# Kernel optimization log

Measured on AMD Instinct MI355X. Metric: run time of the kernel, lower is better.

The kernel has to match this reference:

```python
import jax, jax.numpy as jnp
import numpy as np


def setup_inputs() -> dict:
    key = jax.random.key(0)
    k1, k2, k3, k4 = jax.random.split(key, 4)
    B, S, D = 8, 2048, 512
    scale = 1.0 / np.sqrt(D)
    return {
        "x": jax.random.normal(k1, (B, S, D), dtype=jnp.float32),
        "WQ": jax.random.normal(k2, (D, D), dtype=jnp.float32) * scale,
        "WK": jax.random.normal(k3, (D, D), dtype=jnp.float32) * scale,
        "WV": jax.random.normal(k4, (D, D), dtype=jnp.float32) * scale,
    }


def reference(x, WQ, WK, WV):
    # x: [B, S, D]; single-head scaled dot-product self-attention
    Q = jnp.einsum("bsd,de->bse", x, WQ)
    K = jnp.einsum("bsd,de->bse", x, WK)
    V = jnp.einsum("bsd,de->bse", x, WV)
    d_k = jnp.asarray(K.shape[-1], dtype=x.dtype)
    scores = jnp.einsum("bqd,bkd->bqk", Q, K) / jnp.sqrt(d_k)  # [B,S,S]
    weights = jax.nn.softmax(scores, axis=-1)
    return jnp.einsum("bqk,bkd->bqd", weights, V)
```

## Files before the change

### kernel.cpp

```cpp
#include <hip/hip_runtime.h>
#include <cstdint>
#include <cstddef>

#define B_ 8
#define S_ 2048
#define D_ 512

typedef float f32x4 __attribute__((ext_vector_type(4)));
typedef __bf16 bf16x8 __attribute__((ext_vector_type(8)));

__device__ __forceinline__ unsigned short f2bf(float f) {
    unsigned u = __builtin_bit_cast(unsigned, f);
    u += 0x7FFFu + ((u >> 16) & 1u);
    return (unsigned short)(u >> 16);
}

__device__ __forceinline__ void gll16(const void* g, void* l) {
    __builtin_amdgcn_global_load_lds(
        (const __attribute__((address_space(1))) unsigned int*)g,
        (__attribute__((address_space(3))) unsigned int*)l, 16, 0, 0);
}

#define VMCNT(n) asm volatile("s_waitcnt vmcnt(%0)" :: "i"(n) : "memory")
#define SBAR()   __builtin_amdgcn_s_barrier()
#define SCHED0() __builtin_amdgcn_sched_barrier(0)

template<int AMT, int BNT>
__global__ __launch_bounds__(512, 2) void gemm8(
    const unsigned short* __restrict__ A,
    const unsigned short* __restrict__ B,
    void* __restrict__ Cv,
    unsigned short* __restrict__ Cv2,
    float* __restrict__ rs_part,
    int K, int lda, int ldb, int ldc,
    long long sA, long long sB, long long sC,
    float scale, int mode, int ntn, int nbatch)
{
    constexpr int BM     = 64 * AMT;
    constexpr int BN     = 128 * BNT;
    constexpr int ABYTES = BM * 128;
    constexpr int BBYTES = BN * 128;
    constexpr int AH     = ABYTES / 2;
    constexpr int BH     = BBYTES / 2;
    constexpr int AGL    = AMT / 2;
    constexpr int BGL    = BNT;
    constexpr int BUFB   = ABYTES + BBYTES;
    __shared__ __align__(16) char lds[2 * BUFB];

    const int lin = blockIdx.x;
    const int bz  = lin % nbatch;
    const int tq  = lin / nbatch;
    const int tn  = tq % ntn;
    const int tm  = tq / ntn;
    A += (long long)bz * sA;
    B += (long long)bz * sB;
    const int m0   = tm * BM;
    const int n0   = tn * BN;
    const int tid  = threadIdx.x;
    const int lane = tid & 63;
    const int w    = tid >> 6;
    const int g2   = w >> 2;
    const int nb   = w & 3;

    const int lrow = lane >> 3;
    const int swz  = ((lane & 7) ^ lrow) << 3;
    const unsigned short* gA[2][AGL];
    const unsigned short* gB[2][BGL];
    #pragma unroll
    for (int h = 0; h < 2; ++h) {
        #pragma unroll
        for (int i = 0; i < AGL; ++i)
            gA[h][i] = A + (size_t)(m0 + h * (BM / 2) + (w * AGL + i) * 8 + lrow) * lda + swz;
        #pragma unroll
        for (int i = 0; i < BGL; ++i)
            gB[h][i] = B + (size_t)(n0 + h * (BN / 2) + (w * BGL + i) * 8 + lrow) * ldb + swz;
    }
    auto stA = [&](int bs, int h, int kof) {
        #pragma unroll
        for (int i = 0; i < AGL; ++i)
            gll16(gA[h][i] + kof, lds + bs * BUFB + h * AH + (w * AGL + i) * 1024);
    };
    auto stB = [&](int bs, int h, int kof) {
        #pragma unroll
        for (int i = 0; i < BGL; ++i)
            gll16(gB[h][i] + kof, lds + bs * BUFB + ABYTES + h * BH + (w * BGL + i) * 1024);
    };

    const int fr = lane & 15;
    const int gq = lane >> 4;
    const int c0 = (gq ^ (fr & 7)) << 4;
    int aoff[AMT], boff[BNT];
    #pragma unroll
    for (int ml = 0; ml < AMT; ++ml)
        aoff[ml] = (g2 * (16 * AMT) + ml * 16 + fr) * 128 + c0;
    #pragma unroll
    for (int nl = 0; nl < BNT; ++nl)
        boff[nl] = (nb * (16 * BNT) + nl * 16 + fr) * 128 + c0;

    bf16x8 af[2 * AMT], bLO[2 * BNT], bHI[2 * BNT];
    f32x4 acc[2 * AMT][2 * BNT] = {};

    auto ldA = [&](const char* Ab, int mh) {
        #pragma unroll
        for (int ml = 0; ml < AMT; ++ml)
            #pragma unroll
            for (int kk = 0; kk < 2; ++kk)
                af[ml * 2 + kk] = *(const bf16x8*)(Ab + mh * AH + (aoff[ml] ^ (kk << 6)));
    };
    auto ldB = [&](const char* Bb, int nh, bf16x8* bf) {
        #pragma unroll
        for (int nl = 0; nl < BNT; ++nl)
            #pragma unroll
            for (int kk = 0; kk < 2; ++kk)
                bf[nl * 2 + kk] = *(const bf16x8*)(Bb + nh * BH + (boff[nl] ^ (kk << 6)));
    };
    auto mma = [&](int mh, int nh, const bf16x8* bf) {
        __builtin_amdgcn_s_setprio(1);
        #pragma unroll
        for (int ml = 0; ml < AMT; ++ml)
            #pragma unroll
            for (int nl = 0; nl < BNT; ++nl)
                #pragma unroll
                for (int kk = 0; kk < 2; ++kk)
                    acc[mh * AMT + ml][nh * BNT + nl] =
                        __builtin_amdgcn_mfma_f32_16x16x32_bf16(
                            af[ml * 2 + kk], bf[nl * 2 + kk],
                            acc[mh * AMT + ml][nh * BNT + nl], 0, 0, 0);
        __builtin_amdgcn_s_setprio(0);
    };

    stA(0, 0, 0);  stB(0, 0, 0);
    stA(0, 1, 0);  stB(0, 1, 0);
    stA(1, 0, 64); stB(1, 0, 64);

    const int NT = K >> 6;
    for (int tt = 0; tt < NT; ++tt) {
        const int bs = tt & 1;
        const char* Ab = lds + bs * BUFB;
        const char* Bb = Ab + ABYTES;
        const bool last = (tt == NT - 1);

        if (!last) stA(bs ^ 1, 1, (tt + 1) << 6);
        if (last) { VMCNT(AGL + BGL); } else { VMCNT(6); }
        __builtin_amdgcn_s_barrier();
        SCHED0();
        ldA(Ab, 0); ldB(Bb, 0, bLO);
        mma(0, 0, bLO);

        if (!last) stB(bs ^ 1, 1, (tt + 1) << 6);
        if (last) { VMCNT(0); } else { VMCNT(6); }
        __builtin_amdgcn_s_barrier();
        SCHED0();
        ldB(Bb, 1, bHI);
        mma(0, 1, bHI);

        if (tt + 2 < NT) stA(bs, 0, (tt + 2) << 6);
        VMCNT(6);
        __builtin_amdgcn_s_barrier();
        SCHED0();
        ldA(Ab, 1);
        mma(1, 0, bLO);

        if (tt + 2 < NT) stB(bs, 0, (tt + 2) << 6);
        VMCNT(6);
        __builtin_amdgcn_s_barrier();
        SCHED0();
        mma(1, 1, bHI);
    }

    const int rb4 = gq << 2;
#define AB_(mt) ((((mt) / AMT) * (BM / 2)) + g2 * (16 * AMT) + ((mt) % AMT) * 16)
#define BB_(nt) ((((nt) / BNT) * (BN / 2)) + nb * (16 * BNT) + ((nt) % BNT) * 16)

    if (mode == 3) {
        if (tn >= 4) {
            #pragma unroll
            for (int mt = 0; mt < 2 * AMT; ++mt) {
                const int s0q = m0 + AB_(mt) + rb4;
                const int b   = s0q >> 11;
                const int se  = s0q & (S_ - 1);
                #pragma unroll
                for (int nt = 0; nt < 2 * BNT; ++nt) {
                    const int d = (n0 - 2 * D_) + BB_(nt) + fr;
                    ushort4 u;
                    u.x = f2bf(acc[mt][nt][0]);
                    u.y = f2bf(acc[mt][nt][1]);
                    u.z = f2bf(acc[mt][nt][2]);
                    u.w = f2bf(acc[mt][nt][3]);
                    *(ushort4*)&Cv2[((size_t)b * D_ + d) * S_ + se] = u;
                }
            }
        } else {
            unsigned short* C = (unsigned short*)Cv;
            #pragma unroll
            for (int mt = 0; mt < 2 * AMT; ++mt)
                #pragma unroll
                for (int nt = 0; nt < 2 * BNT; ++nt) {
                    const int gc = n0 + BB_(nt) + fr;
                    #pragma unroll
                    for (int r = 0; r < 4; ++r)
                        C[(size_t)(m0 + AB_(mt) + rb4 + r) * ldc + gc] = f2bf(acc[mt][nt][r]);
                }
        }
    }
#undef AB_
#undef BB_
}

__global__ __launch_bounds__(512, 2) void fused_attn(
    const unsigned short* __restrict__ qk,
    const unsigned short* __restrict__ vtb,
    float* __restrict__ out,
    float scale)
{
    __shared__ __align__(16) char lds[115712];
    char* const PB = lds + 98304;
    float* const RS = (float*)(lds + 114688);

    const int lin = blockIdx.x;
    const int bz  = lin & 7;
    const int q0  = (lin >> 3) * 64;
    const int tid = threadIdx.x;
    const int lane = tid & 63;
    const int w   = tid >> 6;
    const int fr  = lane & 15;
    const int gq  = lane >> 4;
    const int g2  = w >> 2;
    const int nb  = w & 3;

    int row4[4], sc4[4];
    #pragma unroll
    for (int i = 0; i < 4; ++i) {
        const int off = tid * 16 + i * 8192;
        row4[i] = off >> 8;
        sc4[i]  = ((((off >> 4) & 15) ^ (row4[i] & 7)) << 3);
    }
    const size_t qrowb = (size_t)bz * S_;

    auto stK = [&](int b, int kv0, int j) {
        #pragma unroll
        for (int i = 0; i < 4; ++i)
            gll16(qk + (qrowb + kv0 + row4[i]) * 1024 + 512 + j * 128 + sc4[i],
                  lds + b * 49152 + tid * 16 + i * 8192);
    };
    auto stQ = [&](int b, int j) {
        #pragma unroll
        for (int i = 0; i < 2; ++i)
            gll16(qk + (qrowb + q0 + row4[i]) * 1024 + j * 128 + sc4[i],
                  lds + b * 49152 + 32768 + tid * 16 + i * 8192);
    };
    auto stV = [&](int b, int kv0, int c) {
        #pragma unroll
        for (int i = 0; i < 4; ++i)
            gll16(vtb + ((size_t)bz * D_ + c * 128 + row4[i]) * S_ + kv0 + sc4[i],
                  lds + b * 49152 + tid * 16 + i * 8192);
    };

    f32x4 acc_pv[4][4] = {};
    float rsl = 0.f;
    const int k7 = fr & 7;

    stK(0, 0, 0); stQ(0, 0);
    __syncthreads();
    int cur = 0;

    for (int kvi = 0; kvi < 16; ++kvi) {
        const int kv0 = kvi * 128;

        f32x4 acc_s[4] = {};
        #pragma unroll
        for (int j = 0; j < 4; ++j) {
            if (j < 3) { stK(cur ^ 1, kv0, j + 1); stQ(cur ^ 1, j + 1); }
            else       { stV(cur ^ 1, kv0, 0); }
            const char* Kb = lds + cur * 49152;
            const char* Qb = Kb + 32768;
            #pragma unroll
            for (int kk = 0; kk < 4; ++kk) {
                const int ch = ((kk * 4 + gq) ^ k7) << 4;
                const bf16x8 qf = *(const bf16x8*)(Qb + (nb * 16 + fr) * 256 + ch);
                #pragma unroll
                for (int mt = 0; mt < 4; ++mt) {
                    const bf16x8 kf = *(const bf16x8*)(
                        Kb + (g2 * 64 + mt * 16 + fr) * 256 + ch);
                    acc_s[mt] = __builtin_amdgcn_mfma_f32_16x16x32_bf16(
                        kf, qf, acc_s[mt], 0, 0, 0);
                }
            }
            __syncthreads();
            cur ^= 1;
        }

        #pragma unroll
        for (int mt = 0; mt < 4; ++mt) {
            float p0 = __expf(acc_s[mt][0] * scale);
            float p1 = __expf(acc_s[mt][1] * scale);
            float p2 = __expf(acc_s[mt][2] * scale);
            float p3 = __expf(acc_s[mt][3] * scale);
            rsl += (p0 + p1) + (p2 + p3);
            ushort4 u;
            u.x = f2bf(p0); u.y = f2bf(p1); u.z = f2bf(p2); u.w = f2bf(p3);
            const int chunk = g2 * 8 + mt * 2 + (gq >> 1);
            *(ushort4*)(PB + (nb * 16 + fr) * 256 +
                        ((chunk ^ k7) << 4) + (gq & 1) * 8) = u;
        }
        __syncthreads();

        bf16x8 pf[4][4];
        #pragma unroll
        for (int nt2 = 0; nt2 < 4; ++nt2)
            #pragma unroll
            for (int ks = 0; ks < 4; ++ks)
                pf[nt2][ks] = *(const bf16x8*)(
                    PB + (nt2 * 16 + fr) * 256 + (((ks * 4 + gq) ^ k7) << 4));

        #pragma unroll
        for (int c = 0; c < 4; ++c) {
            if (c < 3)          stV(cur ^ 1, kv0, c + 1);
            else if (kvi < 15) { stK(cur ^ 1, kv0 + 128, 0); stQ(cur ^ 1, 0); }
            const char* Vb = lds + cur * 49152;
            #pragma unroll
            for (int ks = 0; ks < 4; ++ks) {
                const bf16x8 vf = *(const bf16x8*)(
                    Vb + (w * 16 + fr) * 256 + (((ks * 4 + gq) ^ k7) << 4));
                #pragma unroll
                for (int nt2 = 0; nt2 < 4; ++nt2)
                    acc_pv[c][nt2] = __builtin_amdgcn_mfma_f32_16x16x32_bf16(
                        vf, pf[nt2][ks], acc_pv[c][nt2], 0, 0, 0);
            }
            __syncthreads();
            cur ^= 1;
        }
    }

    rsl += __shfl_xor(rsl, 16);
    rsl += __shfl_xor(rsl, 32);
    if (lane < 16) RS[g2 * 64 + nb * 16 + lane] = rsl;
    __syncthreads();

    #pragma unroll
    for (int nt2 = 0; nt2 < 4; ++nt2) {
        const int q = nt2 * 16 + fr;
        const float inv = __builtin_amdgcn_rcpf(RS[q] + RS[64 + q]);
        float* op = out + ((qrowb + q0 + q) * D_);
        #pragma unroll
        for (int c = 0; c < 4; ++c) {
            const int d0 = c * 128 + w * 16 + gq * 4;
            float4 o;
            o.x = acc_pv[c][nt2][0] * inv;
            o.y = acc_pv[c][nt2][1] * inv;
            o.z = acc_pv[c][nt2][2] * inv;
            o.w = acc_pv[c][nt2][3] * inv;
            *(float4*)(op + d0) = o;
        }
    }
}

__global__ __launch_bounds__(256) void convert_x4(const float* __restrict__ x,
                                                  unsigned short* __restrict__ xb) {
    const size_t i = ((size_t)blockIdx.x * 256 + threadIdx.x) * 4;
    const float4 f = *(const float4*)(x + i);
    ushort4 u;
    u.x = f2bf(f.x); u.y = f2bf(f.y); u.z = f2bf(f.z); u.w = f2bf(f.w);
    *(ushort4*)(xb + i) = u;
}

__global__ __launch_bounds__(256) void convert_w(const float* __restrict__ WQ,
                                                 const float* __restrict__ WK,
                                                 const float* __restrict__ WV,
                                                 unsigned short* __restrict__ WT) {
    const int o = blockIdx.x * 256 + threadIdx.x;
    const float* W = blockIdx.y == 0 ? WQ : (blockIdx.y == 1 ? WK : WV);
    const int e = o >> 9, d = o & (D_ - 1);
    WT[(size_t)blockIdx.y * D_ * D_ + o] = f2bf(W[d * D_ + e]);
}

extern "C" void kernel_launch(void* const* d_in, const int* in_sizes, int n_in,
                              void* d_out, int out_size, void* d_ws, size_t ws_size,
                              hipStream_t stream)
{
    const float* x  = (const float*)d_in[0];
    const float* WQ = (const float*)d_in[1];
    const float* WK = (const float*)d_in[2];
    const float* WV = (const float*)d_in[3];

    unsigned short* ws  = (unsigned short*)d_ws;
    const size_t NX = (size_t)B_ * S_ * D_;
    unsigned short* xb  = ws;
    unsigned short* wtb = xb + NX;
    unsigned short* qk  = wtb + 3 * D_ * D_;
    unsigned short* vtb = qk + NX * 2;

    convert_x4<<<dim3((unsigned)(NX / 4 / 256)), 256, 0, stream>>>(x, xb);
    convert_w<<<dim3(D_ * D_ / 256, 3), 256, 0, stream>>>(WQ, WK, WV, wtb);

    gemm8<2, 2><<<dim3(768), 512, 0, stream>>>(
        xb, wtb, qk, vtb, nullptr, D_, D_, D_, 2 * D_,
        0, 0, 0, 1.0f, 3,  6,  1);

    fused_attn<<<dim3(256), 512, 0, stream>>>(
        qk, vtb, (float*)d_out, 0.04419417382415922f);
}
```

Before: 244.7 us.

## Keep Q tile resident in LDS, retile QK^T warps, enlarge projection GEMM tile

The attention kernel now loads the whole 64x512 Q block into LDS once instead of restreaming Q chunks every KV step. It retiles the score MMA so each warp computes a 2x2 set of 16x16 fragments, which means row sums are combined across four partial groups. __syncthreads is replaced with explicit vmcnt/lgkmcnt waits, barriers and MFMA priority hints. The projection GEMM moves to a 256-row tile (AMT=4) with half the blocks and unused parameters dropped. The larger LDS footprint (about 145 KB) may cap occupancy at one block per CU, and the bigger GEMM tile launches fewer blocks.

```diff
diff --git a/kernel.cpp b/kernel.cpp
--- a/kernel.cpp
+++ b/kernel.cpp
@@ -22,6 +22,7 @@
 }
 
 #define VMCNT(n) asm volatile("s_waitcnt vmcnt(%0)" :: "i"(n) : "memory")
+#define LGKM0()  asm volatile("s_waitcnt lgkmcnt(0)" ::: "memory")
 #define SBAR()   __builtin_amdgcn_s_barrier()
 #define SCHED0() __builtin_amdgcn_sched_barrier(0)
 
@@ -31,10 +32,7 @@
     const unsigned short* __restrict__ B,
     void* __restrict__ Cv,
     unsigned short* __restrict__ Cv2,
-    float* __restrict__ rs_part,
-    int K, int lda, int ldb, int ldc,
-    long long sA, long long sB, long long sC,
-    float scale, int mode, int ntn, int nbatch)
+    int K, int lda, int ldb, int ldc, int ntn)
 {
     constexpr int BM     = 64 * AMT;
     constexpr int BN     = 128 * BNT;
@@ -47,13 +45,9 @@
     constexpr int BUFB   = ABYTES + BBYTES;
     __shared__ __align__(16) char lds[2 * BUFB];
 
-    const int lin = blockIdx.x;
-    const int bz  = lin % nbatch;
-    const int tq  = lin / nbatch;
+    const int tq  = blockIdx.x;
     const int tn  = tq % ntn;
     const int tm  = tq / ntn;
-    A += (long long)bz * sA;
-    B += (long long)bz * sB;
     const int m0   = tm * BM;
     const int n0   = tn * BN;
     const int tid  = threadIdx.x;
@@ -142,66 +136,59 @@
 
         if (!last) stA(bs ^ 1, 1, (tt + 1) << 6);
         if (last) { VMCNT(AGL + BGL); } else { VMCNT(6); }
-        __builtin_amdgcn_s_barrier();
-        SCHED0();
+        SBAR(); SCHED0();
         ldA(Ab, 0); ldB(Bb, 0, bLO);
         mma(0, 0, bLO);
 
         if (!last) stB(bs ^ 1, 1, (tt + 1) << 6);
         if (last) { VMCNT(0); } else { VMCNT(6); }
-        __builtin_amdgcn_s_barrier();
-        SCHED0();
+        SBAR(); SCHED0();
         ldB(Bb, 1, bHI);
         mma(0, 1, bHI);
 
         if (tt + 2 < NT) stA(bs, 0, (tt + 2) << 6);
         VMCNT(6);
-        __builtin_amdgcn_s_barrier();
-        SCHED0();
+        SBAR(); SCHED0();
         ldA(Ab, 1);
         mma(1, 0, bLO);
 
         if (tt + 2 < NT) stB(bs, 0, (tt + 2) << 6);
         VMCNT(6);
-        __builtin_amdgcn_s_barrier();
-        SCHED0();
+        SBAR(); SCHED0();
         mma(1, 1, bHI);
     }
 
     const int rb4 = gq << 2;
 #define AB_(mt) ((((mt) / AMT) * (BM / 2)) + g2 * (16 * AMT) + ((mt) % AMT) * 16)
 #define BB_(nt) ((((nt) / BNT) * (BN / 2)) + nb * (16 * BNT) + ((nt) % BNT) * 16)
-
-    if (mode == 3) {
-        if (tn >= 4) {
-            #pragma unroll
-            for (int mt = 0; mt < 2 * AMT; ++mt) {
-                const int s0q = m0 + AB_(mt) + rb4;
-                const int b   = s0q >> 11;
-                const int se  = s0q & (S_ - 1);
+    if (tn >= 4) {
+        #pragma unroll
+        for (int mt = 0; mt < 2 * AMT; ++mt) {
+            const int s0q = m0 + AB_(mt) + rb4;
+            const int b   = s0q >> 11;
+            const int se  = s0q & (S_ - 1);
+            #pragma unroll
+            for (int nt = 0; nt < 2 * BNT; ++nt) {
+                const int d = (n0 - 2 * D_) + BB_(nt) + fr;
+                ushort4 u;
+                u.x = f2bf(acc[mt][nt][0]);
+                u.y = f2bf(acc[mt][nt][1]);
+                u.z = f2bf(acc[mt][nt][2]);
+                u.w = f2bf(acc[mt][nt][3]);
+                *(ushort4*)&Cv2[((size_t)b * D_ + d) * S_ + se] = u;
+            }
+        }
+    } else {
+        unsigned short* C = (unsigned short*)Cv;
+        #pragma unroll
+        for (int mt = 0; mt < 2 * AMT; ++mt)
+            #pragma unroll
+            for (int nt = 0; nt < 2 * BNT; ++nt) {
+                const int gc = n0 + BB_(nt) + fr;
                 #pragma unroll
-                for (int nt = 0; nt < 2 * BNT; ++nt) {
-                    const int d = (n0 - 2 * D_) + BB_(nt) + fr;
-                    ushort4 u;
-                    u.x = f2bf(acc[mt][nt][0]);
-                    u.y = f2bf(acc[mt][nt][1]);
-                    u.z = f2bf(acc[mt][nt][2]);
-                    u.w = f2bf(acc[mt][nt][3]);
-                    *(ushort4*)&Cv2[((size_t)b * D_ + d) * S_ + se] = u;
-                }
+                for (int r = 0; r < 4; ++r)
+                    C[(size_t)(m0 + AB_(mt) + rb4 + r) * ldc + gc] = f2bf(acc[mt][nt][r]);
             }
-        } else {
-            unsigned short* C = (unsigned short*)Cv;
-            #pragma unroll
-            for (int mt = 0; mt < 2 * AMT; ++mt)
-                #pragma unroll
-                for (int nt = 0; nt < 2 * BNT; ++nt) {
-                    const int gc = n0 + BB_(nt) + fr;
-                    #pragma unroll
-                    for (int r = 0; r < 4; ++r)
-                        C[(size_t)(m0 + AB_(mt) + rb4 + r) * ldc + gc] = f2bf(acc[mt][nt][r]);
-                }
-        }
     }
 #undef AB_
 #undef BB_
@@ -213,9 +200,11 @@
     float* __restrict__ out,
     float scale)
 {
-    __shared__ __align__(16) char lds[115712];
-    char* const PB = lds + 98304;
-    float* const RS = (float*)(lds + 114688);
+    __shared__ __align__(16) char lds[148480];
+    char* const QL = lds;
+    char* const KV = lds + 65536;
+    char* const PB = lds + 131072;
+    float* const RS = (float*)(lds + 147456);
 
     const int lin = blockIdx.x;
     const int bz  = lin & 7;
@@ -225,8 +214,9 @@
     const int w   = tid >> 6;
     const int fr  = lane & 15;
     const int gq  = lane >> 4;
-    const int g2  = w >> 2;
-    const int nb  = w & 3;
+    const int g4  = w >> 1;
+    const int qh  = w & 1;
+    const int k7  = fr & 7;
 
     int row4[4], sc4[4];
     #pragma unroll
@@ -241,69 +231,80 @@
         #pragma unroll
         for (int i = 0; i < 4; ++i)
             gll16(qk + (qrowb + kv0 + row4[i]) * 1024 + 512 + j * 128 + sc4[i],
-                  lds + b * 49152 + tid * 16 + i * 8192);
-    };
-    auto stQ = [&](int b, int j) {
-        #pragma unroll
-        for (int i = 0; i < 2; ++i)
-            gll16(qk + (qrowb + q0 + row4[i]) * 1024 + j * 128 + sc4[i],
-                  lds + b * 49152 + 32768 + tid * 16 + i * 8192);
+                  KV + b * 32768 + tid * 16 + i * 8192);
     };
     auto stV = [&](int b, int kv0, int c) {
         #pragma unroll
         for (int i = 0; i < 4; ++i)
             gll16(vtb + ((size_t)bz * D_ + c * 128 + row4[i]) * S_ + kv0 + sc4[i],
-                  lds + b * 49152 + tid * 16 + i * 8192);
+                  KV + b * 32768 + tid * 16 + i * 8192);
+    };
+    auto stQall = [&]() {
+        #pragma unroll
+        for (int i = 0; i < 8; ++i) {
+            const int off = tid * 16 + i * 8192;
+            const int row = off >> 10;
+            const int cl  = (off >> 4) & 63;
+            const int cp  = (cl & 56) | ((cl & 7) ^ (row & 7));
+            gll16(qk + (qrowb + q0 + row) * 1024 + cp * 8, QL + off);
+        }
     };
 
     f32x4 acc_pv[4][4] = {};
-    float rsl = 0.f;
-    const int k7 = fr & 7;
-
-    stK(0, 0, 0); stQ(0, 0);
-    __syncthreads();
+    float rs0 = 0.f, rs1 = 0.f;
+
+    stQall(); stK(0, 0, 0);
     int cur = 0;
 
     for (int kvi = 0; kvi < 16; ++kvi) {
         const int kv0 = kvi * 128;
-
-        f32x4 acc_s[4] = {};
+        f32x4 acc_s[2][2] = {};
+
         #pragma unroll
         for (int j = 0; j < 4; ++j) {
-            if (j < 3) { stK(cur ^ 1, kv0, j + 1); stQ(cur ^ 1, j + 1); }
-            else       { stV(cur ^ 1, kv0, 0); }
-            const char* Kb = lds + cur * 49152;
-            const char* Qb = Kb + 32768;
+            VMCNT(0);
+            SBAR(); SCHED0();
+            if (j < 3) stK(cur ^ 1, kv0, j + 1);
+            else       stV(cur ^ 1, kv0, 0);
+            const char* Kb = KV + cur * 32768;
+            __builtin_amdgcn_s_setprio(1);
             #pragma unroll
             for (int kk = 0; kk < 4; ++kk) {
                 const int ch = ((kk * 4 + gq) ^ k7) << 4;
-                const bf16x8 qf = *(const bf16x8*)(Qb + (nb * 16 + fr) * 256 + ch);
-                #pragma unroll
-                for (int mt = 0; mt < 4; ++mt) {
-                    const bf16x8 kf = *(const bf16x8*)(
-                        Kb + (g2 * 64 + mt * 16 + fr) * 256 + ch);
-                    acc_s[mt] = __builtin_amdgcn_mfma_f32_16x16x32_bf16(
-                        kf, qf, acc_s[mt], 0, 0, 0);
-                }
+                const bf16x8 kf0 = *(const bf16x8*)(Kb + (g4 * 32 + fr) * 256 + ch);
+                const bf16x8 kf1 = *(const bf16x8*)(Kb + (g4 * 32 + 16 + fr) * 256 + ch);
+                const int cl = j * 16 + kk * 4 + gq;
+                const int cp = ((cl & 56) | ((cl & 7) ^ k7)) << 4;
+                const bf16x8 qf0 = *(const bf16x8*)(QL + (qh * 32 + fr) * 1024 + cp);
+                const bf16x8 qf1 = *(const bf16x8*)(QL + (qh * 32 + 16 + fr) * 1024 + cp);
+                acc_s[0][0] = __builtin_amdgcn_mfma_f32_16x16x32_bf16(kf0, qf0, acc_s[0][0], 0, 0, 0);
+                acc_s[0][1] = __builtin_amdgcn_mfma_f32_16x16x32_bf16(kf0, qf1, acc_s[0][1], 0, 0, 0);
+                acc_s[1][0] = __builtin_amdgcn_mfma_f32_16x16x32_bf16(kf1, qf0, acc_s[1][0], 0, 0, 0);
+                acc_s[1][1] = __builtin_amdgcn_mfma_f32_16x16x32_bf16(kf1, qf1, acc_s[1][1], 0, 0, 0);
             }
-            __syncthreads();
+            __builtin_amdgcn_s_setprio(0);
             cur ^= 1;
         }
 
         #pragma unroll
-        for (int mt = 0; mt < 4; ++mt) {
-            float p0 = __expf(acc_s[mt][0] * scale);
-            float p1 = __expf(acc_s[mt][1] * scale);
-            float p2 = __expf(acc_s[mt][2] * scale);
-            float p3 = __expf(acc_s[mt][3] * scale);
-            rsl += (p0 + p1) + (p2 + p3);
-            ushort4 u;
-            u.x = f2bf(p0); u.y = f2bf(p1); u.z = f2bf(p2); u.w = f2bf(p3);
-            const int chunk = g2 * 8 + mt * 2 + (gq >> 1);
-            *(ushort4*)(PB + (nb * 16 + fr) * 256 +
-                        ((chunk ^ k7) << 4) + (gq & 1) * 8) = u;
-        }
-        __syncthreads();
+        for (int mt = 0; mt < 2; ++mt)
+            #pragma unroll
+            for (int qf = 0; qf < 2; ++qf) {
+                float p0 = __expf(acc_s[mt][qf][0] * scale);
+                float p1 = __expf(acc_s[mt][qf][1] * scale);
+                float p2 = __expf(acc_s[mt][qf][2] * scale);
+                float p3 = __expf(acc_s[mt][qf][3] * scale);
+                if (qf == 0) rs0 += (p0 + p1) + (p2 + p3);
+                else         rs1 += (p0 + p1) + (p2 + p3);
+                ushort4 u;
+                u.x = f2bf(p0); u.y = f2bf(p1); u.z = f2bf(p2); u.w = f2bf(p3);
+                const int row   = qh * 32 + qf * 16 + fr;
+                const int chunk = g4 * 4 + mt * 2 + (gq >> 1);
+                *(ushort4*)(PB + row * 256 + ((chunk ^ k7) << 4) + (gq & 1) * 8) = u;
+            }
+        VMCNT(0);
+        LGKM0();
+        SBAR(); SCHED0();
 
         bf16x8 pf[4][4];
         #pragma unroll
@@ -315,9 +316,11 @@
 
         #pragma unroll
         for (int c = 0; c < 4; ++c) {
+            if (c > 0) { VMCNT(0); SBAR(); SCHED0(); }
             if (c < 3)          stV(cur ^ 1, kv0, c + 1);
-            else if (kvi < 15) { stK(cur ^ 1, kv0 + 128, 0); stQ(cur ^ 1, 0); }
-            const char* Vb = lds + cur * 49152;
+            else if (kvi < 15)  stK(cur ^ 1, kv0 + 128, 0);
+            const char* Vb = KV + cur * 32768;
+            __builtin_amdgcn_s_setprio(1);
             #pragma unroll
             for (int ks = 0; ks < 4; ++ks) {
                 const bf16x8 vf = *(const bf16x8*)(
@@ -327,20 +330,24 @@
                     acc_pv[c][nt2] = __builtin_amdgcn_mfma_f32_16x16x32_bf16(
                         vf, pf[nt2][ks], acc_pv[c][nt2], 0, 0, 0);
             }
-            __syncthreads();
+            __builtin_amdgcn_s_setprio(0);
             cur ^= 1;
         }
     }
 
-    rsl += __shfl_xor(rsl, 16);
-    rsl += __shfl_xor(rsl, 32);
-    if (lane < 16) RS[g2 * 64 + nb * 16 + lane] = rsl;
+    rs0 += __shfl_xor(rs0, 16); rs0 += __shfl_xor(rs0, 32);
+    rs1 += __shfl_xor(rs1, 16); rs1 += __shfl_xor(rs1, 32);
+    if (lane < 16) {
+        RS[g4 * 64 + qh * 32 + lane]      = rs0;
+        RS[g4 * 64 + qh * 32 + 16 + lane] = rs1;
+    }
     __syncthreads();
 
     #pragma unroll
     for (int nt2 = 0; nt2 < 4; ++nt2) {
         const int q = nt2 * 16 + fr;
-        const float inv = __builtin_amdgcn_rcpf(RS[q] + RS[64 + q]);
+        const float inv = __builtin_amdgcn_rcpf(
+            (RS[q] + RS[64 + q]) + (RS[128 + q] + RS[192 + q]));
         float* op = out + ((qrowb + q0 + q) * D_);
         #pragma unroll
         for (int c = 0; c < 4; ++c) {
@@ -393,9 +400,8 @@
     convert_x4<<<dim3((unsigned)(NX / 4 / 256)), 256, 0, stream>>>(x, xb);
     convert_w<<<dim3(D_ * D_ / 256, 3), 256, 0, stream>>>(WQ, WK, WV, wtb);
 
-    gemm8<2, 2><<<dim3(768), 512, 0, stream>>>(
-        xb, wtb, qk, vtb, nullptr, D_, D_, D_, 2 * D_,
-        0, 0, 0, 1.0f, 3,  6,  1);
+    gemm8<4, 2><<<dim3(384), 512, 0, stream>>>(
+        xb, wtb, qk, vtb, D_, D_, D_, 2 * D_,  6);
 
     fused_attn<<<dim3(256), 512, 0, stream>>>(
         qk, vtb, (float*)d_out, 0.04419417382415922f);
```

After: 230.6 us. -5.7%, faster.
